# Performance work log

Measured on AMD Instinct MI355X. Metric: run time of the kernel, lower is better.

Reference implementation:

```python
import jax, jax.numpy as jnp
import numpy as np

MIN_FP16 = float(np.finfo(np.float16).min)  # -65504.0, matches torch.finfo(torch.float16).min


def _apply_rotary(x, cos, sin):
    # x: [B, H, S, D]; cos/sin: [S, D//2]
    # Equivalent to view_as_complex on interleaved pairs, multiply by freq_cis, view_as_real.
    xr = x[..., 0::2]
    xi = x[..., 1::2]
    c = cos[None, None]  # [1,1,S,D//2]
    s = sin[None, None]
    out_r = xr * c - xi * s
    out_i = xr * s + xi * c
    return jnp.stack([out_r, out_i], axis=-1).reshape(x.shape)


def setup_inputs() -> dict:
    key = jax.random.key(0)
    ks = jax.random.split(key, 4)
    B, S, D_MODEL, H = 2, 2048, 1024, 16
    HS = D_MODEL // H  # 64
    x = jax.random.normal(ks[0], (B, S, D_MODEL), dtype=jnp.float32)
    # Standard RoPE frequencies: theta_i = 10000^(-2i/HS)
    inv_freq = 1.0 / (10000.0 ** (np.arange(0, HS, 2, dtype=np.float32) / HS))  # [HS//2]
    t = np.arange(S, dtype=np.float32)
    angles = np.outer(t, inv_freq)  # [S, HS//2]
    cos = jnp.asarray(np.cos(angles))
    sin = jnp.asarray(np.sin(angles))
    mask = jnp.tril(jnp.ones((S, S), dtype=jnp.int32))[None, None]  # [1,1,S,S] causal
    scale = 1.0 / np.sqrt(D_MODEL)
    W_proj = jax.random.normal(ks[1], (D_MODEL, 3 * D_MODEL), dtype=jnp.float32) * scale
    b_proj = jnp.zeros((3 * D_MODEL,), dtype=jnp.float32)
    W_ff = jax.random.normal(ks[2], (D_MODEL, D_MODEL), dtype=jnp.float32) * scale
    b_ff = jnp.zeros((D_MODEL,), dtype=jnp.float32)
    return {"x": x, "cos_q": cos, "sin_q": sin, "cos_k": cos, "sin_k": sin,
            "mask": mask, "W_proj": W_proj, "b_proj": b_proj, "W_ff": W_ff, "b_ff": b_ff}


def reference(x, cos_q, sin_q, cos_k, sin_k, mask, W_proj, b_proj, W_ff, b_ff):
    B, S, d_model = x.shape
    H = 16
    HS = d_model // H
    head_scale = jnp.sqrt(jnp.float32(HS))

    # fused QKV projection, then split: [B,S,3*dm] -> [3,B,H,S,HS]
    x_proj = x @ W_proj + b_proj
    x_proj = x_proj.reshape(B, S, 3, H, HS).transpose(2, 0, 3, 1, 4)
    q, k, v = x_proj[0], x_proj[1], x_proj[2]

    # mask path: cache pre-RoPE k,v
    next_prefix_kv = jnp.stack([k, v])  # [2,B,H,S,HS]

    q = _apply_rotary(q, cos_q, sin_q)
    k = _apply_rotary(k, cos_k, sin_k)

    scores = jnp.einsum('bhqd,bhkd->bhqk', q, k) / head_scale
    scores = jnp.where(mask == 0, jnp.float32(MIN_FP16), scores)
    probs = jax.nn.softmax(scores, axis=-1)
    attn_o = jnp.einsum('bhqk,bhkd->bhqd', probs, v)  # [B,H,S,HS]

    attn_o = attn_o.transpose(0, 2, 1, 3).reshape(B, S, d_model)
    ff_o = attn_o @ W_ff + b_ff
    return ff_o, next_prefix_kv
```

## Files before the change

### kernel.cpp

```cpp
#include <hip/hip_runtime.h>
#include <stdint.h>

#define DM    1024
#define NH    16
#define HS    64
#define S_LEN 2048

typedef short bf16x8 __attribute__((ext_vector_type(8)));
typedef float f32x4  __attribute__((ext_vector_type(4)));
typedef unsigned short u16x4 __attribute__((ext_vector_type(4)));

__device__ __forceinline__ uint16_t f2b(float f) {
    union { float f; uint32_t i; } x; x.f = f;
    uint32_t r = x.i + 0x7fffu + ((x.i >> 16) & 1u);
    return (uint16_t)(r >> 16);
}
__device__ __forceinline__ uint32_t pack2(float a, float b) {
    return (uint32_t)f2b(a) | ((uint32_t)f2b(b) << 16);
}
__device__ __forceinline__ f32x4 mfma16(bf16x8 a, bf16x8 b, f32x4 c) {
    return __builtin_amdgcn_mfma_f32_16x16x32_bf16(a, b, c, 0, 0, 0);
}
__device__ __forceinline__ float fast_exp2(float x) {
    return __builtin_amdgcn_exp2f(x);
}
template<int CTRL>
__device__ __forceinline__ float dpp_max(float x) {
    union { float f; int i; } u; u.f = x;
    int y = __builtin_amdgcn_update_dpp(u.i, u.i, CTRL, 0xF, 0xF, true);
    union { int i; float f; } v; v.i = y;
    return fmaxf(x, v.f);
}

__device__ __forceinline__ void transpose_tile(
    const float* __restrict__ W, uint16_t* __restrict__ WT, int N,
    int n0, int k0, float (*T)[33])
{
    const int tx = threadIdx.x & 31, ty = threadIdx.x >> 5;
    #pragma unroll
    for (int i = 0; i < 4; ++i)
        T[ty + i * 8][tx] = W[(size_t)(k0 + ty + i * 8) * N + n0 + tx];
    __syncthreads();
    #pragma unroll
    for (int i = 0; i < 4; ++i)
        WT[(size_t)(n0 + ty + i * 8) * 1024 + k0 + tx] = f2b(T[tx][ty + i * 8]);
}

__global__ __launch_bounds__(256) void prep(
    const float* __restrict__ x, uint16_t* __restrict__ xbf,
    const float* __restrict__ Wp, uint16_t* __restrict__ WpT)
{
    __shared__ float T[32][33];
    const int blk = blockIdx.x;
    if (blk < 3072) {
        transpose_tile(Wp, WpT, 3072, (blk % 96) * 32, (blk / 96) * 32, T);
    } else {
        const size_t i = (size_t)(blk - 3072) * 256 + threadIdx.x;
        const float4* p = (const float4*)x + i * 2;
        float4 a = p[0], b = p[1];
        uint4 o;
        o.x = pack2(a.x, a.y); o.y = pack2(a.z, a.w);
        o.z = pack2(b.x, b.y); o.w = pack2(b.z, b.w);
        ((uint4*)xbf)[i] = o;
    }
}

__global__ __launch_bounds__(256) void transpose_w(
    const float* __restrict__ W, uint16_t* __restrict__ WT, int N)
{
    __shared__ float T[32][33];
    transpose_tile(W, WT, N, blockIdx.x * 32, blockIdx.y * 32, T);
}

#define LOADK(K0, A_, B_)                                                                  \
    do {                                                                                   \
        if (ABF) {                                                                         \
            const uint16_t* ap_ = (const uint16_t*)Araw + (size_t)(m0 + sm) * 1024 + (K0) + skc; \
            A_ = *(const uint4*)ap_;                                                       \
        } else {                                                                           \
            const float* ap_ = (const float*)Araw + (size_t)(m0 + sm) * 1024 + (K0) + skc; \
            float4 f0_ = *(const float4*)(ap_ + 0),  f1_ = *(const float4*)(ap_ + 4);      \
            A_.x = pack2(f0_.x, f0_.y); A_.y = pack2(f0_.z, f0_.w);                        \
            A_.z = pack2(f1_.x, f1_.y); A_.w = pack2(f1_.z, f1_.w);                        \
        }                                                                                  \
        const uint16_t* bp_ = BT + (size_t)(n0 + sm) * 1024 + (K0) + skc;                  \
        B_ = *(const uint4*)bp_;                                                           \
    } while (0)

#define STOREK(BUF, A_, B_)                                                                \
    do {                                                                                   \
        *(uint4*)&As[BUF][sm][skc] = A_;                                                   \
        *(uint4*)&Bs[BUF][sm][skc] = B_;                                                   \
    } while (0)

#define COMPUTEK(BUF)                                                                      \
    do {                                                                                   \
        bf16x8 af_[2], bf_[4];                                                             \
        _Pragma("unroll")                                                                  \
        for (int mi = 0; mi < 2; ++mi)                                                     \
            af_[mi] = *(const bf16x8*)&As[BUF][wm + mi * 16 + li][quad * 8];               \
        _Pragma("unroll")                                                                  \
        for (int ni = 0; ni < 4; ++ni)                                                     \
            bf_[ni] = *(const bf16x8*)&Bs[BUF][wn + ni * 16 + li][quad * 8];               \
        _Pragma("unroll")                                                                  \
        for (int mi = 0; mi < 2; ++mi)                                                     \
            _Pragma("unroll")                                                              \
            for (int ni = 0; ni < 4; ++ni)                                                 \
                acc[mi][ni] = mfma16(af_[mi], bf_[ni], acc[mi][ni]);                       \
    } while (0)

#define STAGE_GLL(BUF, K0)                                                                 \
    do {                                                                                   \
        const uint16_t* ga_ = (const uint16_t*)Araw +                                      \
            (size_t)(m0 + wave * 16 + (lane >> 2)) * 1024 + (K0) + (lane & 3) * 8;         \
        __builtin_amdgcn_global_load_lds(                                                  \
            (const __attribute__((address_space(1))) void*)ga_,                            \
            (__attribute__((address_space(3))) void*)&As[BUF][wave * 16][0], 16, 0, 0);    \
        const uint16_t* gb_ = BT +                                                         \
            (size_t)(n0 + wave * 16 + (lane >> 2)) * 1024 + (K0) + (lane & 3) * 8;         \
        __builtin_amdgcn_global_load_lds(                                                  \
            (const __attribute__((address_space(1))) void*)gb_,                            \
            (__attribute__((address_space(3))) void*)&Bs[BUF][wave * 16][0], 16, 0, 0);    \
    } while (0)

template<int MODE, bool ABF, bool WV>
__global__ __launch_bounds__(512) void gemm_mfma(
    const void* __restrict__ Araw,
    const uint16_t* __restrict__ BT,
    const float* __restrict__ bias,
    int N,
    const float* __restrict__ cq, const float* __restrict__ sq,
    const float* __restrict__ ck, const float* __restrict__ sk,
    uint16_t* __restrict__ qbuf, uint16_t* __restrict__ kbuf,
    float* __restrict__ kout, float* __restrict__ vout,
    uint16_t* __restrict__ vtb,
    float* __restrict__ Cout)
{
    __shared__ uint16_t As[2][128][32];
    __shared__ uint16_t Bs[2][128][32];

    const int tid  = threadIdx.x;
    const int wave = tid >> 6, lane = tid & 63;
    const int quad = lane >> 4, li = lane & 15;
    const int wm = (wave >> 1) * 32, wn = (wave & 1) * 64;
    const int m0 = blockIdx.y * 128, n0 = blockIdx.x * 128;

    f32x4 acc[2][4];
    #pragma unroll
    for (int a = 0; a < 2; ++a)
        #pragma unroll
        for (int c = 0; c < 4; ++c)
            acc[a][c] = (f32x4){0.f, 0.f, 0.f, 0.f};

    const int sm = tid >> 2, skc = (tid & 3) * 8;

    if constexpr (ABF) {
        STAGE_GLL(0, 0);
        __syncthreads();
        for (int t = 0; t < 32; t += 2) {
            if (t + 1 < 32) STAGE_GLL(1, (t + 1) * 32);
            COMPUTEK(0);
            __syncthreads();
            if (t + 2 < 32) STAGE_GLL(0, (t + 2) * 32);
            COMPUTEK(1);
            __syncthreads();
        }
    } else {
        uint4 Aa, Ba, Ab, Bb;
        LOADK(0, Aa, Ba);
        STOREK(0, Aa, Ba);
        LOADK(32, Ab, Bb);
        __syncthreads();
        for (int t = 0; t < 16; ++t) {
            const int kb = t * 64;
            if (t < 15) LOADK(kb + 64, Aa, Ba);
            COMPUTEK(0);
            STOREK(1, Ab, Bb);
            __syncthreads();
            if (t < 15) LOADK(kb + 96, Ab, Bb);
            COMPUTEK(1);
            if (t < 15) {
                STOREK(0, Aa, Ba);
                __syncthreads();
            }
        }
    }

    if (MODE == 1) {
        #pragma unroll
        for (int ni = 0; ni < 4; ++ni) {
            const int n = n0 + wn + ni * 16 + li;
            const float bb = bias[n];
            #pragma unroll
            for (int mi = 0; mi < 2; ++mi)
                #pragma unroll
                for (int r = 0; r < 4; ++r) {
                    const int m = m0 + wm + mi * 16 + quad * 4 + r;
                    Cout[(size_t)m * N + n] = acc[mi][ni][r] + bb;
                }
        }
    } else {
        #pragma unroll
        for (int ni = 0; ni < 4; ++ni) {
            const int n   = n0 + wn + ni * 16 + li;
            const int sel = n >> 10;
            const int d   = n & 1023;
            const int h   = d >> 6;
            const int hd  = d & 63;
            const int i0  = hd >> 1;
            const float bb = bias[n];
            #pragma unroll
            for (int mi = 0; mi < 2; ++mi) {
                const int mb = m0 + wm + mi * 16 + quad * 4;
                const int b  = mb >> 11;
                const int s0 = mb & 2047;
                float vv[4];
                #pragma unroll
                for (int r = 0; r < 4; ++r) {
                    const int s = s0 + r;
                    const float val  = acc[mi][ni][r] + bb;
                    const float part = __shfl_xor(val, 1);
                    const size_t idx = ((size_t)(b * NH + h) * S_LEN + s) * HS + hd;
                    if (sel == 0) {
                        float c = cq[s * 32 + i0], sn = sq[s * 32 + i0];
                        float o = (hd & 1) ? (part * sn + val * c) : (val * c - part * sn);
                        qbuf[idx] = f2b(o * 0.18033688f);
                    } else if (sel == 1) {
                        kout[idx] = val;
                        float c = ck[s * 32 + i0], sn = sk[s * 32 + i0];
                        float o = (hd & 1) ? (part * sn + val * c) : (val * c - part * sn);
                        kbuf[idx] = f2b(o);
                    } else {
                        vout[idx] = val;
                        vv[r] = val;
                    }
                }
                if (WV && sel == 2) {
                    u16x4 u;
                    u[0] = f2b(vv[0]); u[1] = f2b(vv[1]);
                    u[2] = f2b(vv[2]); u[3] = f2b(vv[3]);
                    *(u16x4*)&vtb[((size_t)(b * NH + h) * HS + hd) * S_LEN + s0] = u;
                }
            }
        }
    }
}

__global__ __launch_bounds__(256) void attn_mfma(
    const uint16_t* __restrict__ qbuf,
    const uint16_t* __restrict__ kbuf,
    const uint16_t* __restrict__ vtb,
    uint16_t* __restrict__ obuf)
{
    __shared__ uint16_t Ks[64][72];
    __shared__ uint16_t Vt[64][72];
    __shared__ uint16_t Ps[64][68];

    const int i  = blockIdx.x;
    const int bh = i >> 4;
    const int pr = i & 15;
    const int h = bh & 15, b = bh >> 4;
    const int tid = threadIdx.x;
    const int wave = tid >> 6, lane = tid & 63;
    const int quad = lane >> 4, li = lane & 15;
    const int wrow0 = wave * 16;

    const short onebf = (short)0x3F80;
    const bf16x8 kOnes = {onebf, onebf, onebf, onebf, onebf, onebf, onebf, onebf};

    const int row = tid >> 2, c = (tid & 3) * 16;
    uint4 kr0, kr1, vr0, vr1;

    auto load_kv = [&](int kt) {
        const uint16_t* kp = kbuf + ((size_t)bh * S_LEN + kt * 64 + row) * HS + c;
        kr0 = *(const uint4*)kp;
        kr1 = *(const uint4*)(kp + 8);
        const uint16_t* vp = vtb + ((size_t)bh * HS + row) * S_LEN + kt * 64 + c;
        vr0 = *(const uint4*)vp;
        vr1 = *(const uint4*)(vp + 8);
    };
    load_kv(0);

    for (int tt = 0; tt < 2; ++tt) {
        const int qt = tt ? (31 - pr) : pr;

        const uint16_t* qp = qbuf + ((size_t)bh * S_LEN + qt * 64 + wrow0 + li) * HS + quad * 8;
        const bf16x8 aq0 = *(const bf16x8*)qp;
        const bf16x8 aq1 = *(const bf16x8*)(qp + 32);

        f32x4 oacc[4];
        float m_i[4], l_i[4];
        #pragma unroll
        for (int r = 0; r < 4; ++r) {
            m_i[r] = -1e30f; l_i[r] = 0.f;
            oacc[r] = (f32x4){0.f, 0.f, 0.f, 0.f};
        }

        for (int kt = 0; kt <= qt; ++kt) {
            __syncthreads();
            *(uint4*)&Ks[row][c]     = kr0;
            *(uint4*)&Ks[row][c + 8] = kr1;
            *(uint4*)&Vt[row][c]     = vr0;
            *(uint4*)&Vt[row][c + 8] = vr1;
            __syncthreads();
            if (kt < qt)       load_kv(kt + 1);
            else if (tt == 0)  load_kv(0);

            f32x4 sacc[4];
            __builtin_amdgcn_s_setprio(1);
            #pragma unroll
            for (int ni = 0; ni < 4; ++ni) {
                bf16x8 b0 = *(const bf16x8*)&Ks[ni * 16 + li][quad * 8];
                bf16x8 b1 = *(const bf16x8*)&Ks[ni * 16 + li][32 + quad * 8];
                f32x4 z = (f32x4){0.f, 0.f, 0.f, 0.f};
                z = mfma16(aq0, b0, z);
                sacc[ni] = mfma16(aq1, b1, z);
            }
            __builtin_amdgcn_s_setprio(0);

            const bool diag = (kt == qt);
            float p[4][4];
            #pragma unroll
            for (int ni = 0; ni < 4; ++ni)
                #pragma unroll
                for (int r = 0; r < 4; ++r) {
                    float v = sacc[ni][r];
                    if (diag && (ni * 16 + li > wrow0 + quad * 4 + r)) v = -65504.f;
                    p[ni][r] = v;
                }
            float alp[4];
            #pragma unroll
            for (int r = 0; r < 4; ++r) {
                float mx = fmaxf(fmaxf(p[0][r], p[1][r]), fmaxf(p[2][r], p[3][r]));
                mx = dpp_max<0xB1>(mx);
                mx = dpp_max<0x4E>(mx);
                mx = dpp_max<0x124>(mx);
                mx = dpp_max<0x128>(mx);
                float mnew  = fmaxf(m_i[r], mx);
                alp[r] = fast_exp2(m_i[r] - mnew);
                m_i[r] = mnew;
                #pragma unroll
                for (int ni = 0; ni < 4; ++ni)
                    p[ni][r] = fast_exp2(p[ni][r] - mnew);
                #pragma unroll
                for (int ni = 0; ni < 4; ++ni) oacc[ni][r] *= alp[r];
            }

            #pragma unroll
            for (int ni = 0; ni < 4; ++ni)
                #pragma unroll
                for (int r = 0; r < 4; ++r)
                    Ps[wrow0 + quad * 4 + r][ni * 16 + li] = f2b(p[ni][r]);

            bf16x8 pa0 = *(const bf16x8*)&Ps[wrow0 + li][quad * 8];
            bf16x8 pa1 = *(const bf16x8*)&Ps[wrow0 + li][32 + quad * 8];

            __builtin_amdgcn_s_setprio(1);
            f32x4 ls = (f32x4){0.f, 0.f, 0.f, 0.f};
            ls = mfma16(pa0, kOnes, ls);
            ls = mfma16(pa1, kOnes, ls);

            #pragma unroll
            for (int ni = 0; ni < 4; ++ni) {
                bf16x8 v0 = *(const bf16x8*)&Vt[ni * 16 + li][quad * 8];
                bf16x8 v1 = *(const bf16x8*)&Vt[ni * 16 + li][32 + quad * 8];
                oacc[ni] = mfma16(pa0, v0, oacc[ni]);
                oacc[ni] = mfma16(pa1, v1, oacc[ni]);
            }
            __builtin_amdgcn_s_setprio(0);

            #pragma unroll
            for (int r = 0; r < 4; ++r)
                l_i[r] = l_i[r] * alp[r] + ls[r];
        }

        #pragma unroll
        for (int ni = 0; ni < 4; ++ni)
            #pragma unroll
            for (int r = 0; r < 4; ++r) {
                const int qg = qt * 64 + wrow0 + quad * 4 + r;
                obuf[((size_t)b * S_LEN + qg) * DM + h * HS + ni * 16 + li] =
                    f2b(oacc[ni][r] / l_i[r]);
            }
    }
}

extern "C" void kernel_launch(void* const* d_in, const int* in_sizes, int n_in,
                              void* d_out, int out_size, void* d_ws, size_t ws_size,
                              hipStream_t stream) {
    const float* x  = (const float*)d_in[0];
    const float* cq = (const float*)d_in[1];
    const float* sq = (const float*)d_in[2];
    const float* ck = (const float*)d_in[3];
    const float* sk = (const float*)d_in[4];
    const float* Wp = (const float*)d_in[6];
    const float* bp = (const float*)d_in[7];
    const float* Wf = (const float*)d_in[8];
    const float* bf = (const float*)d_in[9];

    float* out  = (float*)d_out;
    float* ffo  = out;
    float* kout = out + 4194304;
    float* vout = out + 8388608;

    uint16_t* qbuf = (uint16_t*)d_ws;
    uint16_t* kbuf = qbuf + 4194304;
    uint16_t* abuf = kbuf + 4194304;
    uint16_t* vtb  = abuf + 4194304;
    uint16_t* xbf  = vtb  + 4194304;
    uint16_t* WpT  = abuf;
    uint16_t* WfT  = qbuf;

    const bool has_xbf = ws_size >= (size_t)40 * 1024 * 1024;

    dim3 blk(256), blkg(512);
    if (has_xbf) {
        prep<<<dim3(5120), blk, 0, stream>>>(x, xbf, Wp, WpT);
        gemm_mfma<0, true, true><<<dim3(24, 32), blkg, 0, stream>>>(
            xbf, WpT, bp, 3072, cq, sq, ck, sk,
            qbuf, kbuf, kout, vout, vtb, nullptr);
    } else {
        transpose_w<<<dim3(96, 32), blk, 0, stream>>>(Wp, WpT, 3072);
        gemm_mfma<0, false, true><<<dim3(24, 32), blkg, 0, stream>>>(
            x, WpT, bp, 3072, cq, sq, ck, sk,
            qbuf, kbuf, kout, vout, vtb, nullptr);
    }
    attn_mfma<<<dim3(512), blk, 0, stream>>>(qbuf, kbuf, vtb, abuf);
    transpose_w<<<dim3(32, 32), blk, 0, stream>>>(Wf, WfT, 1024);
    gemm_mfma<1, true, false><<<dim3(8, 32), blkg, 0, stream>>>(
        abuf, WfT, bf, 1024, nullptr, nullptr, nullptr, nullptr,
        nullptr, nullptr, nullptr, nullptr, nullptr, ffo);
}
```

Measured before the change: 251.1 us.

## Retile GEMM to 128x64 with K=64 steps and attention to 128-key tiles

The GEMM kernel moves from 512-thread 128x128 blocks with K-step 32 to 256-thread 128x64 blocks with K-step 64, doubling the grid. Each wave now owns a 32x64 tile, and the fp32 fallback path becomes single-buffered. The attention kernel processes 128 keys per iteration instead of 64, halving loop trips and barriers, with the causal mask applied only on the last tile. The aim is fewer synchronisations and deeper MFMA work per stage, at the cost of more LDS and registers and extra masked compute on the diagonal tiles.

```diff
diff --git a/kernel.cpp b/kernel.cpp
--- a/kernel.cpp
+++ b/kernel.cpp
@@ -72,59 +72,52 @@
     transpose_tile(W, WT, N, blockIdx.x * 32, blockIdx.y * 32, T);
 }
 
-#define LOADK(K0, A_, B_)                                                                  \
+#define GLL16(SRC, DST)                                                                    \
+    __builtin_amdgcn_global_load_lds(                                                      \
+        (const __attribute__((address_space(1))) void*)(SRC),                              \
+        (__attribute__((address_space(3))) void*)(DST), 16, 0, 0)
+
+#define STAGE_GLL(BUF, K0)                                                                 \
     do {                                                                                   \
-        if (ABF) {                                                                         \
-            const uint16_t* ap_ = (const uint16_t*)Araw + (size_t)(m0 + sm) * 1024 + (K0) + skc; \
-            A_ = *(const uint4*)ap_;                                                       \
-        } else {                                                                           \
-            const float* ap_ = (const float*)Araw + (size_t)(m0 + sm) * 1024 + (K0) + skc; \
-            float4 f0_ = *(const float4*)(ap_ + 0),  f1_ = *(const float4*)(ap_ + 4);      \
-            A_.x = pack2(f0_.x, f0_.y); A_.y = pack2(f0_.z, f0_.w);                        \
-            A_.z = pack2(f1_.x, f1_.y); A_.w = pack2(f1_.z, f1_.w);                        \
-        }                                                                                  \
-        const uint16_t* bp_ = BT + (size_t)(n0 + sm) * 1024 + (K0) + skc;                  \
-        B_ = *(const uint4*)bp_;                                                           \
-    } while (0)
-
-#define STOREK(BUF, A_, B_)                                                                \
-    do {                                                                                   \
-        *(uint4*)&As[BUF][sm][skc] = A_;                                                   \
-        *(uint4*)&Bs[BUF][sm][skc] = B_;                                                   \
+        const uint16_t* ga_ = (const uint16_t*)Araw +                                      \
+            (size_t)(m0 + wave * 32 + (lane >> 3)) * 1024 + (K0) + (lane & 7) * 8;         \
+        GLL16(ga_,             &As[BUF][wave * 32 +  0][0]);                               \
+        GLL16(ga_ +  8 * 1024, &As[BUF][wave * 32 +  8][0]);                               \
+        GLL16(ga_ + 16 * 1024, &As[BUF][wave * 32 + 16][0]);                               \
+        GLL16(ga_ + 24 * 1024, &As[BUF][wave * 32 + 24][0]);                               \
+        const uint16_t* gb_ = BT +                                                         \
+            (size_t)(n0 + wave * 16 + (lane >> 3)) * 1024 + (K0) + (lane & 7) * 8;         \
+        GLL16(gb_,             &Bs[BUF][wave * 16 + 0][0]);                                 \
+        GLL16(gb_ +  8 * 1024, &Bs[BUF][wave * 16 + 8][0]);                                 \
     } while (0)
 
 #define COMPUTEK(BUF)                                                                      \
     do {                                                                                   \
-        bf16x8 af_[2], bf_[4];                                                             \
+        bf16x8 a0_[2], a1_[2], b0_[4], b1_[4];                                             \
         _Pragma("unroll")                                                                  \
-        for (int mi = 0; mi < 2; ++mi)                                                     \
-            af_[mi] = *(const bf16x8*)&As[BUF][wm + mi * 16 + li][quad * 8];               \
+        for (int mi = 0; mi < 2; ++mi) {                                                   \
+            a0_[mi] = *(const bf16x8*)&As[BUF][wm + mi * 16 + li][quad * 8];               \
+            a1_[mi] = *(const bf16x8*)&As[BUF][wm + mi * 16 + li][32 + quad * 8];          \
+        }                                                                                  \
         _Pragma("unroll")                                                                  \
-        for (int ni = 0; ni < 4; ++ni)                                                     \
-            bf_[ni] = *(const bf16x8*)&Bs[BUF][wn + ni * 16 + li][quad * 8];               \
+        for (int ni = 0; ni < 4; ++ni) {                                                   \
+            b0_[ni] = *(const bf16x8*)&Bs[BUF][ni * 16 + li][quad * 8];                    \
+            b1_[ni] = *(const bf16x8*)&Bs[BUF][ni * 16 + li][32 + quad * 8];               \
+        }                                                                                  \
         _Pragma("unroll")                                                                  \
         for (int mi = 0; mi < 2; ++mi)                                                     \
             _Pragma("unroll")                                                              \
             for (int ni = 0; ni < 4; ++ni)                                                 \
-                acc[mi][ni] = mfma16(af_[mi], bf_[ni], acc[mi][ni]);                       \
+                acc[mi][ni] = mfma16(a0_[mi], b0_[ni], acc[mi][ni]);                       \
+        _Pragma("unroll")                                                                  \
+        for (int mi = 0; mi < 2; ++mi)                                                     \
+            _Pragma("unroll")                                                              \
+            for (int ni = 0; ni < 4; ++ni)                                                 \
+                acc[mi][ni] = mfma16(a1_[mi], b1_[ni], acc[mi][ni]);                       \
     } while (0)
 
-#define STAGE_GLL(BUF, K0)                                                                 \
-    do {                                                                                   \
-        const uint16_t* ga_ = (const uint16_t*)Araw +                                      \
-            (size_t)(m0 + wave * 16 + (lane >> 2)) * 1024 + (K0) + (lane & 3) * 8;         \
-        __builtin_amdgcn_global_load_lds(                                                  \
-            (const __attribute__((address_space(1))) void*)ga_,                            \
-            (__attribute__((address_space(3))) void*)&As[BUF][wave * 16][0], 16, 0, 0);    \
-        const uint16_t* gb_ = BT +                                                         \
-            (size_t)(n0 + wave * 16 + (lane >> 2)) * 1024 + (K0) + (lane & 3) * 8;         \
-        __builtin_amdgcn_global_load_lds(                                                  \
-            (const __attribute__((address_space(1))) void*)gb_,                            \
-            (__attribute__((address_space(3))) void*)&Bs[BUF][wave * 16][0], 16, 0, 0);    \
-    } while (0)
-
 template<int MODE, bool ABF, bool WV>
-__global__ __launch_bounds__(512) void gemm_mfma(
+__global__ __launch_bounds__(256) void gemm_mfma(
     const void* __restrict__ Araw,
     const uint16_t* __restrict__ BT,
     const float* __restrict__ bias,
@@ -136,14 +129,14 @@
     uint16_t* __restrict__ vtb,
     float* __restrict__ Cout)
 {
-    __shared__ uint16_t As[2][128][32];
-    __shared__ uint16_t Bs[2][128][32];
+    __shared__ uint16_t As[2][128][64];
+    __shared__ uint16_t Bs[2][64][64];
 
     const int tid  = threadIdx.x;
     const int wave = tid >> 6, lane = tid & 63;
     const int quad = lane >> 4, li = lane & 15;
-    const int wm = (wave >> 1) * 32, wn = (wave & 1) * 64;
-    const int m0 = blockIdx.y * 128, n0 = blockIdx.x * 128;
+    const int wm = wave * 32;
+    const int m0 = blockIdx.y * 128, n0 = blockIdx.x * 64;
 
     f32x4 acc[2][4];
     #pragma unroll
@@ -152,44 +145,57 @@
         for (int c = 0; c < 4; ++c)
             acc[a][c] = (f32x4){0.f, 0.f, 0.f, 0.f};
 
-    const int sm = tid >> 2, skc = (tid & 3) * 8;
-
     if constexpr (ABF) {
         STAGE_GLL(0, 0);
         __syncthreads();
-        for (int t = 0; t < 32; t += 2) {
-            if (t + 1 < 32) STAGE_GLL(1, (t + 1) * 32);
+        for (int t = 0; t < 16; t += 2) {
+            if (t + 1 < 16) STAGE_GLL(1, (t + 1) * 64);
             COMPUTEK(0);
             __syncthreads();
-            if (t + 2 < 32) STAGE_GLL(0, (t + 2) * 32);
+            if (t + 2 < 16) STAGE_GLL(0, (t + 2) * 64);
             COMPUTEK(1);
             __syncthreads();
         }
     } else {
-        uint4 Aa, Ba, Ab, Bb;
-        LOADK(0, Aa, Ba);
-        STOREK(0, Aa, Ba);
-        LOADK(32, Ab, Bb);
-        __syncthreads();
+        const int ar_ = tid >> 1, ac_ = (tid & 1) * 32;
+        const int br_ = tid >> 2, bc_ = (tid & 3) * 16;
         for (int t = 0; t < 16; ++t) {
-            const int kb = t * 64;
-            if (t < 15) LOADK(kb + 64, Aa, Ba);
+            const int K0 = t * 64;
+            const float* ap_ = (const float*)Araw + (size_t)(m0 + ar_) * 1024 + K0 + ac_;
+            uint4 aw0, aw1, aw2, aw3;
+            {
+                float4 f0 = *(const float4*)(ap_ + 0),  f1 = *(const float4*)(ap_ + 4);
+                float4 f2 = *(const float4*)(ap_ + 8),  f3 = *(const float4*)(ap_ + 12);
+                float4 f4 = *(const float4*)(ap_ + 16), f5 = *(const float4*)(ap_ + 20);
+                float4 f6 = *(const float4*)(ap_ + 24), f7 = *(const float4*)(ap_ + 28);
+                aw0.x = pack2(f0.x, f0.y); aw0.y = pack2(f0.z, f0.w);
+                aw0.z = pack2(f1.x, f1.y); aw0.w = pack2(f1.z, f1.w);
+                aw1.x = pack2(f2.x, f2.y); aw1.y = pack2(f2.z, f2.w);
+                aw1.z = pack2(f3.x, f3.y); aw1.w = pack2(f3.z, f3.w);
+                aw2.x = pack2(f4.x, f4.y); aw2.y = pack2(f4.z, f4.w);
+                aw2.z = pack2(f5.x, f5.y); aw2.w = pack2(f5.z, f5.w);
+                aw3.x = pack2(f6.x, f6.y); aw3.y = pack2(f6.z, f6.w);
+                aw3.z = pack2(f7.x, f7.y); aw3.w = pack2(f7.z, f7.w);
+            }
+            const uint16_t* bp_ = BT + (size_t)(n0 + br_) * 1024 + K0 + bc_;
+            uint4 bw0 = *(const uint4*)bp_;
+            uint4 bw1 = *(const uint4*)(bp_ + 8);
+            __syncthreads();
+            *(uint4*)&As[0][ar_][ac_]      = aw0;
+            *(uint4*)&As[0][ar_][ac_ + 8]  = aw1;
+            *(uint4*)&As[0][ar_][ac_ + 16] = aw2;
+            *(uint4*)&As[0][ar_][ac_ + 24] = aw3;
+            *(uint4*)&Bs[0][br_][bc_]      = bw0;
+            *(uint4*)&Bs[0][br_][bc_ + 8]  = bw1;
+            __syncthreads();
             COMPUTEK(0);
-            STOREK(1, Ab, Bb);
-            __syncthreads();
-            if (t < 15) LOADK(kb + 96, Ab, Bb);
-            COMPUTEK(1);
-            if (t < 15) {
-                STOREK(0, Aa, Ba);
-                __syncthreads();
-            }
         }
     }
 
     if (MODE == 1) {
         #pragma unroll
         for (int ni = 0; ni < 4; ++ni) {
-            const int n = n0 + wn + ni * 16 + li;
+            const int n = n0 + ni * 16 + li;
             const float bb = bias[n];
             #pragma unroll
             for (int mi = 0; mi < 2; ++mi)
@@ -202,7 +208,7 @@
     } else {
         #pragma unroll
         for (int ni = 0; ni < 4; ++ni) {
-            const int n   = n0 + wn + ni * 16 + li;
+            const int n   = n0 + ni * 16 + li;
             const int sel = n >> 10;
             const int d   = n & 1023;
             const int h   = d >> 6;
@@ -252,9 +258,9 @@
     const uint16_t* __restrict__ vtb,
     uint16_t* __restrict__ obuf)
 {
-    __shared__ uint16_t Ks[64][72];
-    __shared__ uint16_t Vt[64][72];
-    __shared__ uint16_t Ps[64][68];
+    __shared__ uint16_t Ks[128][72];
+    __shared__ uint16_t Vt[64][136];
+    __shared__ uint16_t Ps[64][136];
 
     const int i  = blockIdx.x;
     const int bh = i >> 4;
@@ -268,21 +274,23 @@
     const short onebf = (short)0x3F80;
     const bf16x8 kOnes = {onebf, onebf, onebf, onebf, onebf, onebf, onebf, onebf};
 
-    const int row = tid >> 2, c = (tid & 3) * 16;
-    uint4 kr0, kr1, vr0, vr1;
-
-    auto load_kv = [&](int kt) {
-        const uint16_t* kp = kbuf + ((size_t)bh * S_LEN + kt * 64 + row) * HS + c;
-        kr0 = *(const uint4*)kp;
-        kr1 = *(const uint4*)(kp + 8);
-        const uint16_t* vp = vtb + ((size_t)bh * HS + row) * S_LEN + kt * 64 + c;
-        vr0 = *(const uint4*)vp;
-        vr1 = *(const uint4*)(vp + 8);
+    const int krow = tid >> 1, kc = (tid & 1) * 32;
+    const int vrow = tid >> 2, vc = (tid & 3) * 32;
+    uint4 kr0, kr1, kr2, kr3, vr0, vr1, vr2, vr3;
+
+    auto load_kv = [&](int s2) {
+        const uint16_t* kp = kbuf + ((size_t)bh * S_LEN + s2 * 128 + krow) * HS + kc;
+        kr0 = *(const uint4*)kp;         kr1 = *(const uint4*)(kp + 8);
+        kr2 = *(const uint4*)(kp + 16);  kr3 = *(const uint4*)(kp + 24);
+        const uint16_t* vp = vtb + ((size_t)bh * HS + vrow) * S_LEN + s2 * 128 + vc;
+        vr0 = *(const uint4*)vp;         vr1 = *(const uint4*)(vp + 8);
+        vr2 = *(const uint4*)(vp + 16);  vr3 = *(const uint4*)(vp + 24);
     };
     load_kv(0);
 
     for (int tt = 0; tt < 2; ++tt) {
-        const int qt = tt ? (31 - pr) : pr;
+        const int qt  = tt ? (31 - pr) : pr;
+        const int nst = (qt + 2) >> 1;
 
         const uint16_t* qp = qbuf + ((size_t)bh * S_LEN + qt * 64 + wrow0 + li) * HS + quad * 8;
         const bf16x8 aq0 = *(const bf16x8*)qp;
@@ -296,42 +304,52 @@
             oacc[r] = (f32x4){0.f, 0.f, 0.f, 0.f};
         }
 
-        for (int kt = 0; kt <= qt; ++kt) {
-            __syncthreads();
-            *(uint4*)&Ks[row][c]     = kr0;
-            *(uint4*)&Ks[row][c + 8] = kr1;
-            *(uint4*)&Vt[row][c]     = vr0;
-            *(uint4*)&Vt[row][c + 8] = vr1;
-            __syncthreads();
-            if (kt < qt)       load_kv(kt + 1);
+        for (int s = 0; s < nst; ++s) {
+            __syncthreads();
+            *(uint4*)&Ks[krow][kc]      = kr0;
+            *(uint4*)&Ks[krow][kc + 8]  = kr1;
+            *(uint4*)&Ks[krow][kc + 16] = kr2;
+            *(uint4*)&Ks[krow][kc + 24] = kr3;
+            *(uint4*)&Vt[vrow][vc]      = vr0;
+            *(uint4*)&Vt[vrow][vc + 8]  = vr1;
+            *(uint4*)&Vt[vrow][vc + 16] = vr2;
+            *(uint4*)&Vt[vrow][vc + 24] = vr3;
+            __syncthreads();
+            if (s + 1 < nst)   load_kv(s + 1);
             else if (tt == 0)  load_kv(0);
 
-            f32x4 sacc[4];
+            float p[8][4];
             __builtin_amdgcn_s_setprio(1);
             #pragma unroll
-            for (int ni = 0; ni < 4; ++ni) {
-                bf16x8 b0 = *(const bf16x8*)&Ks[ni * 16 + li][quad * 8];
-                bf16x8 b1 = *(const bf16x8*)&Ks[ni * 16 + li][32 + quad * 8];
-                f32x4 z = (f32x4){0.f, 0.f, 0.f, 0.f};
-                z = mfma16(aq0, b0, z);
-                sacc[ni] = mfma16(aq1, b1, z);
-            }
+            for (int hf = 0; hf < 2; ++hf)
+                #pragma unroll
+                for (int ni = 0; ni < 4; ++ni) {
+                    bf16x8 b0 = *(const bf16x8*)&Ks[hf * 64 + ni * 16 + li][quad * 8];
+                    bf16x8 b1 = *(const bf16x8*)&Ks[hf * 64 + ni * 16 + li][32 + quad * 8];
+                    f32x4 z = (f32x4){0.f, 0.f, 0.f, 0.f};
+                    z = mfma16(aq0, b0, z);
+                    z = mfma16(aq1, b1, z);
+                    #pragma unroll
+                    for (int r = 0; r < 4; ++r) p[hf * 4 + ni][r] = z[r];
+                }
             __builtin_amdgcn_s_setprio(0);
 
-            const bool diag = (kt == qt);
-            float p[4][4];
-            #pragma unroll
-            for (int ni = 0; ni < 4; ++ni)
-                #pragma unroll
-                for (int r = 0; r < 4; ++r) {
-                    float v = sacc[ni][r];
-                    if (diag && (ni * 16 + li > wrow0 + quad * 4 + r)) v = -65504.f;
-                    p[ni][r] = v;
+            if (s == nst - 1) {
+                #pragma unroll
+                for (int g = 0; g < 8; ++g) {
+                    const int col = s * 128 + g * 16 + li;
+                    #pragma unroll
+                    for (int r = 0; r < 4; ++r)
+                        if (col > qt * 64 + wrow0 + quad * 4 + r) p[g][r] = -65504.f;
                 }
+            }
+
             float alp[4];
             #pragma unroll
             for (int r = 0; r < 4; ++r) {
-                float mx = fmaxf(fmaxf(p[0][r], p[1][r]), fmaxf(p[2][r], p[3][r]));
+                float mx = p[0][r];
+                #pragma unroll
+                for (int g = 1; g < 8; ++g) mx = fmaxf(mx, p[g][r]);
                 mx = dpp_max<0xB1>(mx);
                 mx = dpp_max<0x4E>(mx);
                 mx = dpp_max<0x124>(mx);
@@ -340,32 +358,40 @@
                 alp[r] = fast_exp2(m_i[r] - mnew);
                 m_i[r] = mnew;
                 #pragma unroll
-                for (int ni = 0; ni < 4; ++ni)
-                    p[ni][r] = fast_exp2(p[ni][r] - mnew);
+                for (int g = 0; g < 8; ++g)
+                    p[g][r] = fast_exp2(p[g][r] - mnew);
                 #pragma unroll
                 for (int ni = 0; ni < 4; ++ni) oacc[ni][r] *= alp[r];
             }
 
             #pragma unroll
-            for (int ni = 0; ni < 4; ++ni)
+            for (int g = 0; g < 8; ++g)
                 #pragma unroll
                 for (int r = 0; r < 4; ++r)
-                    Ps[wrow0 + quad * 4 + r][ni * 16 + li] = f2b(p[ni][r]);
+                    Ps[wrow0 + quad * 4 + r][g * 16 + li] = f2b(p[g][r]);
 
             bf16x8 pa0 = *(const bf16x8*)&Ps[wrow0 + li][quad * 8];
             bf16x8 pa1 = *(const bf16x8*)&Ps[wrow0 + li][32 + quad * 8];
+            bf16x8 pa2 = *(const bf16x8*)&Ps[wrow0 + li][64 + quad * 8];
+            bf16x8 pa3 = *(const bf16x8*)&Ps[wrow0 + li][96 + quad * 8];
 
             __builtin_amdgcn_s_setprio(1);
             f32x4 ls = (f32x4){0.f, 0.f, 0.f, 0.f};
             ls = mfma16(pa0, kOnes, ls);
             ls = mfma16(pa1, kOnes, ls);
+            ls = mfma16(pa2, kOnes, ls);
+            ls = mfma16(pa3, kOnes, ls);
 
             #pragma unroll
             for (int ni = 0; ni < 4; ++ni) {
                 bf16x8 v0 = *(const bf16x8*)&Vt[ni * 16 + li][quad * 8];
                 bf16x8 v1 = *(const bf16x8*)&Vt[ni * 16 + li][32 + quad * 8];
+                bf16x8 v2 = *(const bf16x8*)&Vt[ni * 16 + li][64 + quad * 8];
+                bf16x8 v3 = *(const bf16x8*)&Vt[ni * 16 + li][96 + quad * 8];
                 oacc[ni] = mfma16(pa0, v0, oacc[ni]);
                 oacc[ni] = mfma16(pa1, v1, oacc[ni]);
+                oacc[ni] = mfma16(pa2, v2, oacc[ni]);
+                oacc[ni] = mfma16(pa3, v3, oacc[ni]);
             }
             __builtin_amdgcn_s_setprio(0);
 
@@ -413,21 +439,21 @@
 
     const bool has_xbf = ws_size >= (size_t)40 * 1024 * 1024;
 
-    dim3 blk(256), blkg(512);
+    dim3 blk(256);
     if (has_xbf) {
         prep<<<dim3(5120), blk, 0, stream>>>(x, xbf, Wp, WpT);
-        gemm_mfma<0, true, true><<<dim3(24, 32), blkg, 0, stream>>>(
+        gemm_mfma<0, true, true><<<dim3(48, 32), blk, 0, stream>>>(
             xbf, WpT, bp, 3072, cq, sq, ck, sk,
             qbuf, kbuf, kout, vout, vtb, nullptr);
     } else {
         transpose_w<<<dim3(96, 32), blk, 0, stream>>>(Wp, WpT, 3072);
-        gemm_mfma<0, false, true><<<dim3(24, 32), blkg, 0, stream>>>(
+        gemm_mfma<0, false, true><<<dim3(48, 32), blk, 0, stream>>>(
             x, WpT, bp, 3072, cq, sq, ck, sk,
             qbuf, kbuf, kout, vout, vtb, nullptr);
     }
     attn_mfma<<<dim3(512), blk, 0, stream>>>(qbuf, kbuf, vtb, abuf);
     transpose_w<<<dim3(32, 32), blk, 0, stream>>>(Wf, WfT, 1024);
-    gemm_mfma<1, true, false><<<dim3(8, 32), blkg, 0, stream>>>(
+    gemm_mfma<1, true, false><<<dim3(16, 32), blk, 0, stream>>>(
         abuf, WfT, bf, 1024, nullptr, nullptr, nullptr, nullptr,
         nullptr, nullptr, nullptr, nullptr, nullptr, ffo);
 }
```

After: 244.5 us. -2.7%, faster.
